# Kernel tuning notes

Measured on AMD Instinct MI355X. Metric: run time of the kernel, lower is better.

Reference implementation:

```python
import jax, jax.numpy as jnp
import numpy as np

N, B, H, OUT, T = 200000, 1024, 256, 128, 2  # nodes, graphs, hidden(=in_dim), out_dim, timesteps
NEG_SLOPE = 0.01


def setup_inputs() -> dict:
    key = jax.random.key(0)
    ks = jax.random.split(key, 12)
    s = 0.05
    f32 = jnp.float32
    return {
        "x": jax.random.normal(ks[0], (N, H), dtype=f32),
        "batch": jnp.sort(jax.random.randint(ks[1], (N,), 0, B)),
        # GATConv params (heads=1, shared lin for src/dst since in_channels is int)
        "W": jax.random.normal(ks[2], (H, H), dtype=f32) * s,
        "att_src": jax.random.normal(ks[3], (H,), dtype=f32) * s,
        "att_dst": jax.random.normal(ks[4], (H,), dtype=f32) * s,
        "bias_gat": jnp.zeros((H,), dtype=f32),
        # GRUCell params (input_size = H, hidden_size = H)
        "W_ih": jax.random.normal(ks[5], (3 * H, H), dtype=f32) * s,
        "W_hh": jax.random.normal(ks[6], (3 * H, H), dtype=f32) * s,
        "b_ih": jnp.zeros((3 * H,), dtype=f32),
        "b_hh": jnp.zeros((3 * H,), dtype=f32),
        # final Linear
        "W_lin": jax.random.normal(ks[7], (H, OUT), dtype=f32) * s,
        "b_lin": jnp.zeros((OUT,), dtype=f32),
    }


def reference(x, batch, W, att_src, att_dst, bias_gat, W_ih, W_hh, b_ih, b_hh, W_lin, b_lin):
    # out = global_add_pool(x, batch)  -> [B, H]
    out = jax.ops.segment_sum(x, batch, num_segments=B)
    for _ in range(T):
        # --- bipartite GATConv((x, out), edge_index=[arange(N), batch]) ---
        xs = x @ W                       # [N, H] transformed source nodes
        od = out @ W                     # [B, H] transformed dst (graph) nodes
        a_src = xs @ att_src             # [N]
        a_dst = od @ att_dst             # [B]
        e = a_src + a_dst[batch]         # [N] per-edge raw score (one edge per node)
        e = jnp.where(e > 0, e, NEG_SLOPE * e)  # leaky_relu(negative_slope=0.01)
        # scatter-softmax over each graph's incoming edges
        emax = jax.ops.segment_max(e, batch, num_segments=B)
        ee = jnp.exp(e - emax[batch])
        denom = jax.ops.segment_sum(ee, batch, num_segments=B)
        alpha = ee / denom[batch]        # [N]
        # scatter-add aggregation of weighted messages
        agg = jax.ops.segment_sum(xs * alpha[:, None], batch, num_segments=B) + bias_gat
        h = jax.nn.elu(agg)              # [B, H]  (dropout is identity in eval)
        # --- GRUCell(h, out) ---
        gi = h @ W_ih.T + b_ih           # [B, 3H]
        gh = out @ W_hh.T + b_hh         # [B, 3H]
        r = jax.nn.sigmoid(gi[:, :H] + gh[:, :H])
        z = jax.nn.sigmoid(gi[:, H:2 * H] + gh[:, H:2 * H])
        n = jnp.tanh(gi[:, 2 * H:] + r * gh[:, 2 * H:])
        out = jax.nn.silu((1.0 - z) * n + z * out)  # activation = F.silu
    return out @ W_lin + b_lin           # [B, OUT]
```

## Files before the change

### kernel.cpp

```cpp
#include <hip/hip_runtime.h>
#include <math.h>

#define N_NODES 200000
#define BGRAPH  1024
#define HDIM    256
#define ODIM    128
#define SCAP    1024

typedef __attribute__((ext_vector_type(8))) short short8;

__device__ __forceinline__ unsigned short f2bf(float f) {
    union { float f; unsigned int i; } c; c.f = f;
    unsigned int i = c.i;
    unsigned int r = i + 0x7FFFu + ((i >> 16) & 1u);
    return (unsigned short)(r >> 16);
}
__device__ __forceinline__ float bf2f(unsigned short h) {
    union { unsigned int i; float f; } c; c.i = ((unsigned int)h) << 16;
    return c.f;
}

__global__ __launch_bounds__(256) void k_prep(const float* __restrict__ W,
        const float* __restrict__ att_src, const float* __restrict__ att_dst,
        const int* __restrict__ batch, const float* __restrict__ W_ih,
        const float* __restrict__ W_hh, float* __restrict__ v,
        float* __restrict__ u, int* __restrict__ seg,
        unsigned short* __restrict__ Wg) {
    int t = threadIdx.x;
    if (blockIdx.x < 256) {
        int i = blockIdx.x;
        float w = W[(size_t)i * HDIM + t];
        __shared__ float r1[256], r2[256];
        r1[t] = w * att_src[t];
        r2[t] = w * att_dst[t];
        __syncthreads();
        for (int st = 128; st > 0; st >>= 1) {
            if (t < st) { r1[t] += r1[t + st]; r2[t] += r2[t + st]; }
            __syncthreads();
        }
        if (t == 0) { v[i] = r1[0]; u[i] = r2[0]; }
    } else if (blockIdx.x < 261) {
        int b = (blockIdx.x - 256) * 256 + t;
        if (b > BGRAPH) return;
        if (b == BGRAPH) { seg[b] = N_NODES; return; }
        int lo = 0, hi = N_NODES;
        while (lo < hi) { int mid = (lo + hi) >> 1; if (batch[mid] < b) lo = mid + 1; else hi = mid; }
        seg[b] = lo;
    } else {
        int k = blockIdx.x - 261;
        short8 w8;
        #pragma unroll
        for (int j = 0; j < 3; ++j)
            w8[j] = (short)f2bf(W_ih[(size_t)(j * HDIM + t) * HDIM + k]);
        #pragma unroll
        for (int j = 0; j < 3; ++j)
            w8[3 + j] = (short)f2bf(W_hh[(size_t)(j * HDIM + t) * HDIM + k]);
        w8[6] = 0; w8[7] = 0;
        *(short8*)(Wg + ((size_t)k * HDIM + t) * 8) = w8;
    }
}

__global__ __launch_bounds__(256, 4) void k_fused(const float* __restrict__ x,
        const int* __restrict__ seg, const float* __restrict__ v,
        const float* __restrict__ u, const float* __restrict__ W,
        const float* __restrict__ bias_gat, const unsigned short* __restrict__ Wg,
        const float* __restrict__ b_ih, const float* __restrict__ b_hh,
        const float* __restrict__ W_lin, const float* __restrict__ b_lin,
        float* __restrict__ sfall, float* __restrict__ out) {
    int b = blockIdx.x;
    int lo = seg[b], hi = seg[b + 1];
    int t = threadIdx.x, wave = t >> 6, lane = t & 63;

    __shared__ float s_loc[SCAP];
    __shared__ float comb[4][HDIM];
    __shared__ float red[256];
    __shared__ float axv[HDIM];
    __shared__ float hvec[HDIM];
    __shared__ float oprev[HDIM];
    __shared__ float sred[4], dred[4];

    bool inl = (hi - lo) <= SCAP;
    float ut = u[t];

    float v0 = v[4 * lane + 0], v1 = v[4 * lane + 1];
    float v2 = v[4 * lane + 2], v3 = v[4 * lane + 3];
    float p0 = 0.f, p1 = 0.f, p2 = 0.f, p3 = 0.f;
    float sm = -3.402823466e38f;
    int i = lo + wave;
    for (; i + 4 < hi; i += 8) {
        const float4 r0 = *(const float4*)(x + (size_t)i * HDIM + 4 * lane);
        const float4 r1 = *(const float4*)(x + (size_t)(i + 4) * HDIM + 4 * lane);
        p0 += r0.x + r1.x; p1 += r0.y + r1.y; p2 += r0.z + r1.z; p3 += r0.w + r1.w;
        float pa = r0.x * v0 + r0.y * v1 + r0.z * v2 + r0.w * v3;
        float pb = r1.x * v0 + r1.y * v1 + r1.z * v2 + r1.w * v3;
        #pragma unroll
        for (int off = 32; off > 0; off >>= 1) {
            pa += __shfl_down(pa, off, 64);
            pb += __shfl_down(pb, off, 64);
        }
        if (lane == 0) {
            if (inl) { s_loc[i - lo] = pa; s_loc[i + 4 - lo] = pb; }
            else     { sfall[i] = pa; sfall[i + 4] = pb; }
            sm = fmaxf(sm, fmaxf(pa, pb));
        }
    }
    for (; i < hi; i += 4) {
        const float4 r0 = *(const float4*)(x + (size_t)i * HDIM + 4 * lane);
        p0 += r0.x; p1 += r0.y; p2 += r0.z; p3 += r0.w;
        float pa = r0.x * v0 + r0.y * v1 + r0.z * v2 + r0.w * v3;
        #pragma unroll
        for (int off = 32; off > 0; off >>= 1) pa += __shfl_down(pa, off, 64);
        if (lane == 0) {
            if (inl) s_loc[i - lo] = pa; else sfall[i] = pa;
            sm = fmaxf(sm, pa);
        }
    }
    comb[wave][4 * lane + 0] = p0; comb[wave][4 * lane + 1] = p1;
    comb[wave][4 * lane + 2] = p2; comb[wave][4 * lane + 3] = p3;
    if (lane == 0) sred[wave] = sm;
    __syncthreads();
    float st0 = comb[0][t] + comb[1][t] + comb[2][t] + comb[3][t];
    oprev[t] = st0;
    float smx = fmaxf(fmaxf(sred[0], sred[1]), fmaxf(sred[2], sred[3]));
    red[t] = st0 * ut;
    __syncthreads();
    for (int st = 128; st > 0; st >>= 1) { if (t < st) red[t] += red[t + st]; __syncthreads(); }
    float d = red[0];
    __syncthreads();

    for (int step = 0; step < 2; ++step) {
        float M = smx + d;
        M = M > 0.f ? M : 0.01f * M;

        float a0 = 0.f, a1 = 0.f, a2 = 0.f, a3 = 0.f, den = 0.f;
        i = lo + wave;
        for (; i + 12 < hi; i += 16) {
            float s0v = inl ? s_loc[i - lo]      : sfall[i];
            float s1v = inl ? s_loc[i + 4 - lo]  : sfall[i + 4];
            float s2v = inl ? s_loc[i + 8 - lo]  : sfall[i + 8];
            float s3v = inl ? s_loc[i + 12 - lo] : sfall[i + 12];
            float e0 = s0v + d; e0 = e0 > 0.f ? e0 : 0.01f * e0;
            float e1 = s1v + d; e1 = e1 > 0.f ? e1 : 0.01f * e1;
            float e2 = s2v + d; e2 = e2 > 0.f ? e2 : 0.01f * e2;
            float e3 = s3v + d; e3 = e3 > 0.f ? e3 : 0.01f * e3;
            float w0 = __expf(e0 - M), w1 = __expf(e1 - M);
            float w2 = __expf(e2 - M), w3 = __expf(e3 - M);
            const float4 r0 = *(const float4*)(x + (size_t)i * HDIM + 4 * lane);
            const float4 r1 = *(const float4*)(x + (size_t)(i + 4) * HDIM + 4 * lane);
            const float4 r2 = *(const float4*)(x + (size_t)(i + 8) * HDIM + 4 * lane);
            const float4 r3 = *(const float4*)(x + (size_t)(i + 12) * HDIM + 4 * lane);
            den += (w0 + w1) + (w2 + w3);
            a0 += w0 * r0.x + w1 * r1.x + w2 * r2.x + w3 * r3.x;
            a1 += w0 * r0.y + w1 * r1.y + w2 * r2.y + w3 * r3.y;
            a2 += w0 * r0.z + w1 * r1.z + w2 * r2.z + w3 * r3.z;
            a3 += w0 * r0.w + w1 * r1.w + w2 * r2.w + w3 * r3.w;
        }
        for (; i < hi; i += 4) {
            float s0v = inl ? s_loc[i - lo] : sfall[i];
            float e0 = s0v + d; e0 = e0 > 0.f ? e0 : 0.01f * e0;
            float w0 = __expf(e0 - M);
            const float4 r0 = *(const float4*)(x + (size_t)i * HDIM + 4 * lane);
            den += w0;
            a0 += w0 * r0.x; a1 += w0 * r0.y; a2 += w0 * r0.z; a3 += w0 * r0.w;
        }
        comb[wave][4 * lane + 0] = a0; comb[wave][4 * lane + 1] = a1;
        comb[wave][4 * lane + 2] = a2; comb[wave][4 * lane + 3] = a3;
        if (lane == 0) dred[wave] = den;
        __syncthreads();
        float dtot = dred[0] + dred[1] + dred[2] + dred[3];
        float inv = (hi > lo) ? 1.0f / dtot : 0.f;
        axv[t] = (comb[0][t] + comb[1][t] + comb[2][t] + comb[3][t]) * inv;
        __syncthreads();

        float acc = bias_gat[t];
        #pragma unroll 8
        for (int ii = 0; ii < HDIM; ++ii) acc += axv[ii] * W[(size_t)ii * HDIM + t];
        float hval = acc > 0.f ? acc : expm1f(acc);
        __syncthreads();
        hvec[t] = hval;
        __syncthreads();

        float gr = 0.f, gz = 0.f, gn = 0.f, hr = 0.f, hz = 0.f, hn = 0.f;
        for (int k0 = 0; k0 < HDIM; k0 += 4) {
            float hq[4], oq[4];
            *(float4*)hq = *(const float4*)&hvec[k0];
            *(float4*)oq = *(const float4*)&oprev[k0];
            #pragma unroll
            for (int j = 0; j < 4; ++j) {
                short8 wv = *(const short8*)(Wg + ((size_t)(k0 + j) * HDIM + t) * 8);
                gr += hq[j] * bf2f((unsigned short)wv[0]);
                gz += hq[j] * bf2f((unsigned short)wv[1]);
                gn += hq[j] * bf2f((unsigned short)wv[2]);
                hr += oq[j] * bf2f((unsigned short)wv[3]);
                hz += oq[j] * bf2f((unsigned short)wv[4]);
                hn += oq[j] * bf2f((unsigned short)wv[5]);
            }
        }
        float gir = gr + b_ih[t];
        float giz = gz + b_ih[HDIM + t];
        float gin = gn + b_ih[2 * HDIM + t];
        float ghr = hr + b_hh[t];
        float ghz = hz + b_hh[HDIM + t];
        float ghn = hn + b_hh[2 * HDIM + t];
        float rg = 1.f / (1.f + __expf(-(gir + ghr)));
        float zg = 1.f / (1.f + __expf(-(giz + ghz)));
        float ng = tanhf(gin + rg * ghn);
        float prev = oprev[t];
        float h2 = (1.f - zg) * ng + zg * prev;
        float no = h2 / (1.f + __expf(-h2));
        __syncthreads();
        oprev[t] = no;
        red[t] = no * ut;
        __syncthreads();
        for (int st = 128; st > 0; st >>= 1) { if (t < st) red[t] += red[t + st]; __syncthreads(); }
        d = red[0];
        __syncthreads();
    }

    int half = t >> 7, o = t & 127;
    float acc = 0.f;
    #pragma unroll 8
    for (int k = 0; k < 128; ++k)
        acc += oprev[half * 128 + k] * W_lin[(size_t)(half * 128 + k) * ODIM + o];
    red[t] = acc;
    __syncthreads();
    if (t < 128)
        out[(size_t)b * ODIM + t] = red[t] + red[t + 128] + b_lin[t];
}

extern "C" void kernel_launch(void* const* d_in, const int* in_sizes, int n_in,
                              void* d_out, int out_size, void* d_ws, size_t ws_size,
                              hipStream_t stream) {
    const float* x        = (const float*)d_in[0];
    const int*   batch    = (const int*)d_in[1];
    const float* W        = (const float*)d_in[2];
    const float* att_src  = (const float*)d_in[3];
    const float* att_dst  = (const float*)d_in[4];
    const float* bias_gat = (const float*)d_in[5];
    const float* W_ih     = (const float*)d_in[6];
    const float* W_hh     = (const float*)d_in[7];
    const float* b_ih     = (const float*)d_in[8];
    const float* b_hh     = (const float*)d_in[9];
    const float* W_lin    = (const float*)d_in[10];
    const float* b_lin    = (const float*)d_in[11];

    char* ws = (char*)d_ws;
    size_t off = 0;
    auto alloc = [&](size_t bytes) {
        void* p = (void*)(ws + off);
        off += (bytes + 255) & ~(size_t)255;
        return p;
    };
    int*            seg   = (int*)alloc((BGRAPH + 1) * 4);
    float*          vv    = (float*)alloc(HDIM * 4);
    float*          uu    = (float*)alloc(HDIM * 4);
    float*          sfall = (float*)alloc((size_t)N_NODES * 4);
    unsigned short* Wg    = (unsigned short*)alloc((size_t)HDIM * HDIM * 8 * 2);

    hipLaunchKernelGGL(k_prep, dim3(517), dim3(256), 0, stream,
                       W, att_src, att_dst, batch, W_ih, W_hh, vv, uu, seg, Wg);
    hipLaunchKernelGGL(k_fused, dim3(BGRAPH), dim3(256), 0, stream,
                       x, seg, vv, uu, W, bias_gat, Wg, b_ih, b_hh,
                       W_lin, b_lin, sfall, (float*)d_out);
}
```

Baseline: 444.4 us.

## Use 512-thread blocks, split GEMVs over k, pack GRU and GAT weights as bf16

Doubles the fused kernel's block to 8 waves, so node streaming uses 8 waves per graph and the dense GEMVs (W, GRU, W_lin) are split across the k dimension with a shared-memory combine step. The GRU weights are repacked from 16-byte padded short8 records into 12-byte packed bf16 pairs, and W is now converted to bf16 pairs instead of being read in fp32. The aim is more memory-level parallelism on the x stream and less weight traffic per block. The cost is extra barriers and reductions, and the additional bf16 rounding of W changes numerics.

Result: slower. 794.5 us (+78.8%).

```diff
diff --git a/kernel.cpp b/kernel.cpp
--- a/kernel.cpp
+++ b/kernel.cpp
@@ -7,17 +7,17 @@
 #define ODIM    128
 #define SCAP    1024
 
-typedef __attribute__((ext_vector_type(8))) short short8;
-
 __device__ __forceinline__ unsigned short f2bf(float f) {
     union { float f; unsigned int i; } c; c.f = f;
     unsigned int i = c.i;
     unsigned int r = i + 0x7FFFu + ((i >> 16) & 1u);
     return (unsigned short)(r >> 16);
 }
-__device__ __forceinline__ float bf2f(unsigned short h) {
-    union { unsigned int i; float f; } c; c.i = ((unsigned int)h) << 16;
-    return c.f;
+__device__ __forceinline__ float bflo(unsigned int u) {
+    union { unsigned int i; float f; } c; c.i = u << 16; return c.f;
+}
+__device__ __forceinline__ float bfhi(unsigned int u) {
+    union { unsigned int i; float f; } c; c.i = u & 0xffff0000u; return c.f;
 }
 
 __global__ __launch_bounds__(256) void k_prep(const float* __restrict__ W,
@@ -25,7 +25,7 @@
         const int* __restrict__ batch, const float* __restrict__ W_ih,
         const float* __restrict__ W_hh, float* __restrict__ v,
         float* __restrict__ u, int* __restrict__ seg,
-        unsigned short* __restrict__ Wg) {
+        unsigned int* __restrict__ Wgu, unsigned int* __restrict__ Wpk) {
     int t = threadIdx.x;
     if (blockIdx.x < 256) {
         int i = blockIdx.x;
@@ -46,50 +46,56 @@
         int lo = 0, hi = N_NODES;
         while (lo < hi) { int mid = (lo + hi) >> 1; if (batch[mid] < b) lo = mid + 1; else hi = mid; }
         seg[b] = lo;
+    } else if (blockIdx.x < 517) {
+        int k = blockIdx.x - 261;
+        unsigned int a0 = f2bf(W_ih[(size_t)(0 * HDIM + t) * HDIM + k]);
+        unsigned int a1 = f2bf(W_ih[(size_t)(1 * HDIM + t) * HDIM + k]);
+        unsigned int a2 = f2bf(W_ih[(size_t)(2 * HDIM + t) * HDIM + k]);
+        unsigned int a3 = f2bf(W_hh[(size_t)(0 * HDIM + t) * HDIM + k]);
+        unsigned int a4 = f2bf(W_hh[(size_t)(1 * HDIM + t) * HDIM + k]);
+        unsigned int a5 = f2bf(W_hh[(size_t)(2 * HDIM + t) * HDIM + k]);
+        unsigned int* p = Wgu + ((size_t)k * HDIM + t) * 3;
+        p[0] = a0 | (a1 << 16);
+        p[1] = a2 | (a3 << 16);
+        p[2] = a4 | (a5 << 16);
     } else {
-        int k = blockIdx.x - 261;
-        short8 w8;
-        #pragma unroll
-        for (int j = 0; j < 3; ++j)
-            w8[j] = (short)f2bf(W_ih[(size_t)(j * HDIM + t) * HDIM + k]);
-        #pragma unroll
-        for (int j = 0; j < 3; ++j)
-            w8[3 + j] = (short)f2bf(W_hh[(size_t)(j * HDIM + t) * HDIM + k]);
-        w8[6] = 0; w8[7] = 0;
-        *(short8*)(Wg + ((size_t)k * HDIM + t) * 8) = w8;
-    }
-}
-
-__global__ __launch_bounds__(256, 4) void k_fused(const float* __restrict__ x,
+        int k2 = blockIdx.x - 517;
+        unsigned int lo16 = f2bf(W[(size_t)(2 * k2) * HDIM + t]);
+        unsigned int hi16 = f2bf(W[(size_t)(2 * k2 + 1) * HDIM + t]);
+        Wpk[(size_t)k2 * HDIM + t] = lo16 | (hi16 << 16);
+    }
+}
+
+__global__ __launch_bounds__(512, 8) void k_fused(const float* __restrict__ x,
         const int* __restrict__ seg, const float* __restrict__ v,
-        const float* __restrict__ u, const float* __restrict__ W,
-        const float* __restrict__ bias_gat, const unsigned short* __restrict__ Wg,
+        const float* __restrict__ u, const float* __restrict__ bias_gat,
+        const unsigned int* __restrict__ Wgu, const unsigned int* __restrict__ Wpk,
         const float* __restrict__ b_ih, const float* __restrict__ b_hh,
         const float* __restrict__ W_lin, const float* __restrict__ b_lin,
         float* __restrict__ sfall, float* __restrict__ out) {
     int b = blockIdx.x;
     int lo = seg[b], hi = seg[b + 1];
-    int t = threadIdx.x, wave = t >> 6, lane = t & 63;
+    int t = threadIdx.x, wv = t >> 6, lane = t & 63;
 
     __shared__ float s_loc[SCAP];
-    __shared__ float comb[4][HDIM];
-    __shared__ float red[256];
+    __shared__ float comb[8][HDIM];
+    __shared__ float red[HDIM];
     __shared__ float axv[HDIM];
     __shared__ float hvec[HDIM];
     __shared__ float oprev[HDIM];
-    __shared__ float sred[4], dred[4];
+    __shared__ float sred[8], dred[8];
 
     bool inl = (hi - lo) <= SCAP;
-    float ut = u[t];
+    float ut = u[t & 255];
 
     float v0 = v[4 * lane + 0], v1 = v[4 * lane + 1];
     float v2 = v[4 * lane + 2], v3 = v[4 * lane + 3];
     float p0 = 0.f, p1 = 0.f, p2 = 0.f, p3 = 0.f;
     float sm = -3.402823466e38f;
-    int i = lo + wave;
-    for (; i + 4 < hi; i += 8) {
+    int i = lo + wv;
+    for (; i + 8 < hi; i += 16) {
         const float4 r0 = *(const float4*)(x + (size_t)i * HDIM + 4 * lane);
-        const float4 r1 = *(const float4*)(x + (size_t)(i + 4) * HDIM + 4 * lane);
+        const float4 r1 = *(const float4*)(x + (size_t)(i + 8) * HDIM + 4 * lane);
         p0 += r0.x + r1.x; p1 += r0.y + r1.y; p2 += r0.z + r1.z; p3 += r0.w + r1.w;
         float pa = r0.x * v0 + r0.y * v1 + r0.z * v2 + r0.w * v3;
         float pb = r1.x * v0 + r1.y * v1 + r1.z * v2 + r1.w * v3;
@@ -99,12 +105,12 @@
             pb += __shfl_down(pb, off, 64);
         }
         if (lane == 0) {
-            if (inl) { s_loc[i - lo] = pa; s_loc[i + 4 - lo] = pb; }
-            else     { sfall[i] = pa; sfall[i + 4] = pb; }
+            if (inl) { s_loc[i - lo] = pa; s_loc[i + 8 - lo] = pb; }
+            else     { sfall[i] = pa; sfall[i + 8] = pb; }
             sm = fmaxf(sm, fmaxf(pa, pb));
         }
     }
-    for (; i < hi; i += 4) {
+    for (; i < hi; i += 8) {
         const float4 r0 = *(const float4*)(x + (size_t)i * HDIM + 4 * lane);
         p0 += r0.x; p1 += r0.y; p2 += r0.z; p3 += r0.w;
         float pa = r0.x * v0 + r0.y * v1 + r0.z * v2 + r0.w * v3;
@@ -115,30 +121,37 @@
             sm = fmaxf(sm, pa);
         }
     }
-    comb[wave][4 * lane + 0] = p0; comb[wave][4 * lane + 1] = p1;
-    comb[wave][4 * lane + 2] = p2; comb[wave][4 * lane + 3] = p3;
-    if (lane == 0) sred[wave] = sm;
+    comb[wv][4 * lane + 0] = p0; comb[wv][4 * lane + 1] = p1;
+    comb[wv][4 * lane + 2] = p2; comb[wv][4 * lane + 3] = p3;
+    if (lane == 0) sred[wv] = sm;
     __syncthreads();
-    float st0 = comb[0][t] + comb[1][t] + comb[2][t] + comb[3][t];
-    oprev[t] = st0;
-    float smx = fmaxf(fmaxf(sred[0], sred[1]), fmaxf(sred[2], sred[3]));
-    red[t] = st0 * ut;
+    if (t < HDIM) {
+        float st0 = 0.f;
+        #pragma unroll
+        for (int j = 0; j < 8; ++j) st0 += comb[j][t];
+        oprev[t] = st0;
+        red[t] = st0 * ut;
+    }
+    float smx = fmaxf(fmaxf(fmaxf(sred[0], sred[1]), fmaxf(sred[2], sred[3])),
+                      fmaxf(fmaxf(sred[4], sred[5]), fmaxf(sred[6], sred[7])));
     __syncthreads();
     for (int st = 128; st > 0; st >>= 1) { if (t < st) red[t] += red[t + st]; __syncthreads(); }
     float d = red[0];
     __syncthreads();
 
+    int q = t >> 8, tt = t & 255;
+
     for (int step = 0; step < 2; ++step) {
         float M = smx + d;
         M = M > 0.f ? M : 0.01f * M;
 
         float a0 = 0.f, a1 = 0.f, a2 = 0.f, a3 = 0.f, den = 0.f;
-        i = lo + wave;
-        for (; i + 12 < hi; i += 16) {
+        i = lo + wv;
+        for (; i + 24 < hi; i += 32) {
             float s0v = inl ? s_loc[i - lo]      : sfall[i];
-            float s1v = inl ? s_loc[i + 4 - lo]  : sfall[i + 4];
-            float s2v = inl ? s_loc[i + 8 - lo]  : sfall[i + 8];
-            float s3v = inl ? s_loc[i + 12 - lo] : sfall[i + 12];
+            float s1v = inl ? s_loc[i + 8 - lo]  : sfall[i + 8];
+            float s2v = inl ? s_loc[i + 16 - lo] : sfall[i + 16];
+            float s3v = inl ? s_loc[i + 24 - lo] : sfall[i + 24];
             float e0 = s0v + d; e0 = e0 > 0.f ? e0 : 0.01f * e0;
             float e1 = s1v + d; e1 = e1 > 0.f ? e1 : 0.01f * e1;
             float e2 = s2v + d; e2 = e2 > 0.f ? e2 : 0.01f * e2;
@@ -146,16 +159,16 @@
             float w0 = __expf(e0 - M), w1 = __expf(e1 - M);
             float w2 = __expf(e2 - M), w3 = __expf(e3 - M);
             const float4 r0 = *(const float4*)(x + (size_t)i * HDIM + 4 * lane);
-            const float4 r1 = *(const float4*)(x + (size_t)(i + 4) * HDIM + 4 * lane);
-            const float4 r2 = *(const float4*)(x + (size_t)(i + 8) * HDIM + 4 * lane);
-            const float4 r3 = *(const float4*)(x + (size_t)(i + 12) * HDIM + 4 * lane);
+            const float4 r1 = *(const float4*)(x + (size_t)(i + 8) * HDIM + 4 * lane);
+            const float4 r2 = *(const float4*)(x + (size_t)(i + 16) * HDIM + 4 * lane);
+            const float4 r3 = *(const float4*)(x + (size_t)(i + 24) * HDIM + 4 * lane);
             den += (w0 + w1) + (w2 + w3);
             a0 += w0 * r0.x + w1 * r1.x + w2 * r2.x + w3 * r3.x;
             a1 += w0 * r0.y + w1 * r1.y + w2 * r2.y + w3 * r3.y;
             a2 += w0 * r0.z + w1 * r1.z + w2 * r2.z + w3 * r3.z;
             a3 += w0 * r0.w + w1 * r1.w + w2 * r2.w + w3 * r3.w;
         }
-        for (; i < hi; i += 4) {
+        for (; i < hi; i += 8) {
             float s0v = inl ? s_loc[i - lo] : sfall[i];
             float e0 = s0v + d; e0 = e0 > 0.f ? e0 : 0.01f * e0;
             float w0 = __expf(e0 - M);
@@ -163,69 +176,98 @@
             den += w0;
             a0 += w0 * r0.x; a1 += w0 * r0.y; a2 += w0 * r0.z; a3 += w0 * r0.w;
         }
-        comb[wave][4 * lane + 0] = a0; comb[wave][4 * lane + 1] = a1;
-        comb[wave][4 * lane + 2] = a2; comb[wave][4 * lane + 3] = a3;
-        if (lane == 0) dred[wave] = den;
-        __syncthreads();
-        float dtot = dred[0] + dred[1] + dred[2] + dred[3];
+        comb[wv][4 * lane + 0] = a0; comb[wv][4 * lane + 1] = a1;
+        comb[wv][4 * lane + 2] = a2; comb[wv][4 * lane + 3] = a3;
+        if (lane == 0) dred[wv] = den;
+        __syncthreads();
+        float dtot = (dred[0] + dred[1]) + (dred[2] + dred[3])
+                   + (dred[4] + dred[5]) + (dred[6] + dred[7]);
         float inv = (hi > lo) ? 1.0f / dtot : 0.f;
-        axv[t] = (comb[0][t] + comb[1][t] + comb[2][t] + comb[3][t]) * inv;
-        __syncthreads();
-
-        float acc = bias_gat[t];
-        #pragma unroll 8
-        for (int ii = 0; ii < HDIM; ++ii) acc += axv[ii] * W[(size_t)ii * HDIM + t];
-        float hval = acc > 0.f ? acc : expm1f(acc);
-        __syncthreads();
-        hvec[t] = hval;
+        if (t < HDIM) {
+            float s8 = 0.f;
+            #pragma unroll
+            for (int j = 0; j < 8; ++j) s8 += comb[j][t];
+            axv[t] = s8 * inv;
+        }
+        __syncthreads();
+
+        {
+            float acc = q ? 0.f : bias_gat[tt];
+            int k2e = q * 64 + 64;
+            for (int k2 = q * 64; k2 < k2e; ++k2) {
+                unsigned int w2 = Wpk[(size_t)k2 * HDIM + tt];
+                float2 a2 = *(const float2*)&axv[2 * k2];
+                acc += a2.x * bflo(w2) + a2.y * bfhi(w2);
+            }
+            comb[q][tt] = acc;
+        }
+        __syncthreads();
+        if (t < HDIM) {
+            float hs = comb[0][t] + comb[1][t];
+            hvec[t] = hs > 0.f ? hs : expm1f(hs);
+        }
         __syncthreads();
 
         float gr = 0.f, gz = 0.f, gn = 0.f, hr = 0.f, hz = 0.f, hn = 0.f;
-        for (int k0 = 0; k0 < HDIM; k0 += 4) {
-            float hq[4], oq[4];
-            *(float4*)hq = *(const float4*)&hvec[k0];
-            *(float4*)oq = *(const float4*)&oprev[k0];
-            #pragma unroll
-            for (int j = 0; j < 4; ++j) {
-                short8 wv = *(const short8*)(Wg + ((size_t)(k0 + j) * HDIM + t) * 8);
-                gr += hq[j] * bf2f((unsigned short)wv[0]);
-                gz += hq[j] * bf2f((unsigned short)wv[1]);
-                gn += hq[j] * bf2f((unsigned short)wv[2]);
-                hr += oq[j] * bf2f((unsigned short)wv[3]);
-                hz += oq[j] * bf2f((unsigned short)wv[4]);
-                hn += oq[j] * bf2f((unsigned short)wv[5]);
+        {
+            int k0e = q * 128 + 128;
+            for (int k0 = q * 128; k0 < k0e; k0 += 4) {
+                float hq[4], oq[4];
+                *(float4*)hq = *(const float4*)&hvec[k0];
+                *(float4*)oq = *(const float4*)&oprev[k0];
+                #pragma unroll
+                for (int j = 0; j < 4; ++j) {
+                    const unsigned int* p = Wgu + ((size_t)(k0 + j) * HDIM + tt) * 3;
+                    unsigned int u0 = p[0], u1 = p[1], u2 = p[2];
+                    gr += hq[j] * bflo(u0);
+                    gz += hq[j] * bfhi(u0);
+                    gn += hq[j] * bflo(u1);
+                    hr += oq[j] * bfhi(u1);
+                    hz += oq[j] * bflo(u2);
+                    hn += oq[j] * bfhi(u2);
+                }
             }
         }
-        float gir = gr + b_ih[t];
-        float giz = gz + b_ih[HDIM + t];
-        float gin = gn + b_ih[2 * HDIM + t];
-        float ghr = hr + b_hh[t];
-        float ghz = hz + b_hh[HDIM + t];
-        float ghn = hn + b_hh[2 * HDIM + t];
-        float rg = 1.f / (1.f + __expf(-(gir + ghr)));
-        float zg = 1.f / (1.f + __expf(-(giz + ghz)));
-        float ng = tanhf(gin + rg * ghn);
-        float prev = oprev[t];
-        float h2 = (1.f - zg) * ng + zg * prev;
-        float no = h2 / (1.f + __expf(-h2));
-        __syncthreads();
-        oprev[t] = no;
-        red[t] = no * ut;
+        if (q == 1) {
+            comb[0][tt] = gr; comb[1][tt] = gz; comb[2][tt] = gn;
+            comb[3][tt] = hr; comb[4][tt] = hz; comb[5][tt] = hn;
+        }
+        __syncthreads();
+        if (q == 0) {
+            float gir = gr + comb[0][tt] + b_ih[tt];
+            float giz = gz + comb[1][tt] + b_ih[HDIM + tt];
+            float gin = gn + comb[2][tt] + b_ih[2 * HDIM + tt];
+            float ghr = hr + comb[3][tt] + b_hh[tt];
+            float ghz = hz + comb[4][tt] + b_hh[HDIM + tt];
+            float ghn = hn + comb[5][tt] + b_hh[2 * HDIM + tt];
+            float rg = 1.f / (1.f + __expf(-(gir + ghr)));
+            float zg = 1.f / (1.f + __expf(-(giz + ghz)));
+            float ng = tanhf(gin + rg * ghn);
+            float prev = oprev[tt];
+            float h2 = (1.f - zg) * ng + zg * prev;
+            float no = h2 / (1.f + __expf(-h2));
+            oprev[tt] = no;
+            red[tt] = no * ut;
+        }
         __syncthreads();
         for (int st = 128; st > 0; st >>= 1) { if (t < st) red[t] += red[t + st]; __syncthreads(); }
         d = red[0];
         __syncthreads();
     }
 
-    int half = t >> 7, o = t & 127;
-    float acc = 0.f;
-    #pragma unroll 8
-    for (int k = 0; k < 128; ++k)
-        acc += oprev[half * 128 + k] * W_lin[(size_t)(half * 128 + k) * ODIM + o];
-    red[t] = acc;
+    {
+        int qq = t >> 7, o = t & 127;
+        float acc = 0.f;
+        int ke = qq * 64 + 64;
+        #pragma unroll 8
+        for (int k = qq * 64; k < ke; ++k)
+            acc += oprev[k] * W_lin[(size_t)k * ODIM + o];
+        comb[qq][o] = acc;
+    }
     __syncthreads();
-    if (t < 128)
-        out[(size_t)b * ODIM + t] = red[t] + red[t + 128] + b_lin[t];
+    if (t < ODIM)
+        out[(size_t)b * ODIM + t] = (comb[0][t] + comb[1][t])
+                                  + (comb[2][t] + comb[3][t]) + b_lin[t];
 }
 
 extern "C" void kernel_launch(void* const* d_in, const int* in_sizes, int n_in,
@@ -251,15 +293,16 @@
         off += (bytes + 255) & ~(size_t)255;
         return p;
     };
-    int*            seg   = (int*)alloc((BGRAPH + 1) * 4);
-    float*          vv    = (float*)alloc(HDIM * 4);
-    float*          uu    = (float*)alloc(HDIM * 4);
-    float*          sfall = (float*)alloc((size_t)N_NODES * 4);
-    unsigned short* Wg    = (unsigned short*)alloc((size_t)HDIM * HDIM * 8 * 2);
-
-    hipLaunchKernelGGL(k_prep, dim3(517), dim3(256), 0, stream,
-                       W, att_src, att_dst, batch, W_ih, W_hh, vv, uu, seg, Wg);
-    hipLaunchKernelGGL(k_fused, dim3(BGRAPH), dim3(256), 0, stream,
-                       x, seg, vv, uu, W, bias_gat, Wg, b_ih, b_hh,
+    int*          seg   = (int*)alloc((BGRAPH + 1) * 4);
+    float*        vv    = (float*)alloc(HDIM * 4);
+    float*        uu    = (float*)alloc(HDIM * 4);
+    float*        sfall = (float*)alloc((size_t)N_NODES * 4);
+    unsigned int* Wgu   = (unsigned int*)alloc((size_t)HDIM * HDIM * 3 * 4);
+    unsigned int* Wpk   = (unsigned int*)alloc((size_t)(HDIM / 2) * HDIM * 4);
+
+    hipLaunchKernelGGL(k_prep, dim3(645), dim3(256), 0, stream,
+                       W, att_src, att_dst, batch, W_ih, W_hh, vv, uu, seg, Wgu, Wpk);
+    hipLaunchKernelGGL(k_fused, dim3(BGRAPH), dim3(512), 0, stream,
+                       x, seg, vv, uu, bias_gat, Wgu, Wpk, b_ih, b_hh,
                        W_lin, b_lin, sfall, (float*)d_out);
 }
```
